# Performance work log

Hardware: AMD Instinct MI355X
Metric: run time of the kernel (lower is better)

Reference implementation:

```python
import jax, jax.numpy as jnp
import numpy as np

N_NODES = 100000
N_EDGES = 3200000
N_GRAPHS = 1024
HID = 64
NUM_CLASSES = 21


def setup_inputs() -> dict:
    key = jax.random.key(0)
    ks = jax.random.split(key, 12)
    x = jax.random.normal(ks[0], (N_NODES, 1), dtype=jnp.float32)
    edge_index = jax.random.randint(ks[1], (2, N_EDGES), 0, N_NODES, dtype=jnp.int64)
    batch = jnp.sort(jax.random.randint(ks[2], (N_NODES,), 0, N_GRAPHS, dtype=jnp.int64))
    def lin(k, fan_in, fan_out):
        bound = 1.0 / np.sqrt(fan_in)
        return jax.random.uniform(k, (fan_in, fan_out), jnp.float32, -bound, bound)
    return {
        "x": x,
        "edge_index": edge_index,
        "batch": batch,
        # SAGEConv1: lin_l (on aggregated neighbors, with bias), lin_r (root, no bias)
        "W1l": lin(ks[3], 1, HID), "b1": jnp.zeros((HID,), jnp.float32), "W1r": lin(ks[4], 1, HID),
        # SAGEConv2
        "W2l": lin(ks[5], HID, HID), "b2": jnp.zeros((HID,), jnp.float32), "W2r": lin(ks[6], HID, HID),
        # classifier
        "Wc": lin(ks[7], HID, NUM_CLASSES), "bc": jnp.zeros((NUM_CLASSES,), jnp.float32),
    }


def _sage_conv(x, src, dst, Wl, bl, Wr):
    # mean-aggregate neighbor features: gather from src, scatter-mean to dst
    msg = x[src]                                              # [E, F] gather
    agg = jax.ops.segment_sum(msg, dst, num_segments=N_NODES)  # [N, F]
    cnt = jax.ops.segment_sum(jnp.ones((src.shape[0],), x.dtype), dst, num_segments=N_NODES)
    agg = agg / jnp.maximum(cnt, 1.0)[:, None]
    # out = lin_l(aggr) + lin_r(x)
    return agg @ Wl + bl + x @ Wr


def reference(x, edge_index, batch, W1l, b1, W1r, W2l, b2, W2r, Wc, bc):
    src, dst = edge_index[0], edge_index[1]
    h = jax.nn.relu(_sage_conv(x, src, dst, W1l, b1, W1r))
    h = jax.nn.relu(_sage_conv(h, src, dst, W2l, b2, W2r))
    # global mean pool over graphs
    pooled = jax.ops.segment_sum(h, batch, num_segments=N_GRAPHS)
    gcnt = jax.ops.segment_sum(jnp.ones((h.shape[0],), h.dtype), batch, num_segments=N_GRAPHS)
    pooled = pooled / jnp.maximum(gcnt, 1.0)[:, None]
    return pooled @ Wc + bc
```

## Files before the change

kernel.cpp:

```cpp
#include <hip/hip_runtime.h>

#define N_NODES 100000
#define N_EDGES 3200000
#define N_GRAPHS 1024
#define NCLS 21
#define NBKT 782
#define CAP 4480
#define NB 512
#define CHUNK 6250
#define TROW 72

typedef short s8v __attribute__((ext_vector_type(8)));
typedef float f4v __attribute__((ext_vector_type(4)));

__device__ __forceinline__ float bf2f(unsigned short u) {
    return __uint_as_float(((unsigned)u) << 16);
}
__device__ __forceinline__ unsigned short f2bf(float f) {
    unsigned u = __float_as_uint(f);
    unsigned r = 0x7fffu + ((u >> 16) & 1u);
    return (unsigned short)((u + r) >> 16);
}
__device__ __forceinline__ float lo2f(unsigned w) { return __uint_as_float(w << 16); }
__device__ __forceinline__ float hi2f(unsigned w) { return __uint_as_float(w & 0xffff0000u); }

__global__ void k_prep(const float* __restrict__ W2l, const float* __restrict__ W2r,
                       unsigned short* __restrict__ wp,
                       const int* __restrict__ batch, int* __restrict__ gstart,
                       int* __restrict__ gcur) {
    if (blockIdx.x < 32) {
        int tid = blockIdx.x * 256 + threadIdx.x;
        int frag = tid >> 9;
        int r = tid & 511;
        int L = r >> 3, j = r & 7;
        int kstep = frag >> 2, nt = frag & 3;
        int k = kstep * 32 + (L >> 4) * 8 + j;
        int n = nt * 16 + (L & 15);
        float val = (k < 64) ? W2l[k * 64 + n] : W2r[(k - 64) * 64 + n];
        wp[tid] = f2bf(val);
    } else if (blockIdx.x < 37) {
        int g = (blockIdx.x - 32) * 256 + threadIdx.x;
        if (g > N_GRAPHS) return;
        if (g == N_GRAPHS) { gstart[N_GRAPHS] = N_NODES; return; }
        int lo = 0, hi = N_NODES;
        while (lo < hi) { int m = (lo + hi) >> 1; if (batch[m] < g) lo = m + 1; else hi = m; }
        gstart[g] = lo;
    } else {
        for (int i = threadIdx.x; i < NBKT; i += 256) gcur[i] = i * CAP;
    }
}

__global__ __launch_bounds__(256) void k_binone(const int* __restrict__ src,
                                                const int* __restrict__ dst,
                                                int* __restrict__ gcur,
                                                unsigned int* __restrict__ bins) {
    __shared__ unsigned int ebuf[CHUNK];
    __shared__ unsigned short bbuf[CHUNK];
    __shared__ int lh[NBKT];
    __shared__ int lbase[NBKT];
    int t = threadIdx.x;
    for (int i = t; i < NBKT; i += 256) lh[i] = 0;
    __syncthreads();
    const int2* s2 = (const int2*)(src + blockIdx.x * CHUNK);
    const int2* d2 = (const int2*)(dst + blockIdx.x * CHUNK);
    for (int i = t; i < CHUNK / 2; i += 256) {
        int2 s = s2[i];
        int2 d = d2[i];
        uint2 pp;
        pp.x = ((unsigned)s.x << 7) | (unsigned)(d.x & 127);
        pp.y = ((unsigned)s.y << 7) | (unsigned)(d.y & 127);
        *(uint2*)(&ebuf[2 * i]) = pp;
        bbuf[2 * i]     = (unsigned short)(d.x >> 7);
        bbuf[2 * i + 1] = (unsigned short)(d.y >> 7);
        atomicAdd(&lh[d.x >> 7], 1);
        atomicAdd(&lh[d.y >> 7], 1);
    }
    __syncthreads();
    for (int i = t; i < NBKT; i += 256)
        lbase[i] = atomicAdd(&gcur[i], lh[i]);
    __syncthreads();
    for (int i = t; i < NBKT; i += 256) lh[i] = lbase[i];
    __syncthreads();
    for (int i = t; i < CHUNK; i += 256) {
        int b = (int)bbuf[i];
        int pos = atomicAdd(&lh[b], 1);
        if (pos < (b + 1) * CAP) bins[pos] = ebuf[i];
    }
}

__global__ __launch_bounds__(256) void k_build(
    const int* __restrict__ gcur, unsigned int* __restrict__ bins,
    int* __restrict__ row, unsigned short* __restrict__ deg,
    const float* __restrict__ x,
    const float* __restrict__ W1l, const float* __restrict__ b1,
    const float* __restrict__ W1r, unsigned short* __restrict__ h1b) {
    __shared__ unsigned int ebuf[CAP];
    __shared__ int hist[128];
    __shared__ int curs[128];
    __shared__ int lds[128];
    __shared__ float t1[128];
    int k = blockIdx.x, t = threadIdx.x;
    int e0 = k * CAP;
    int cnt = min(gcur[k] - e0, CAP);
    if (t < 128) { hist[t] = 0; t1[t] = 0.0f; }
    __syncthreads();
    for (int i = t; i < cnt; i += 256) {
        unsigned p = bins[e0 + i];
        ebuf[i] = p;
        atomicAdd(&hist[p & 127u], 1);
    }
    __syncthreads();
    if (t < 128) lds[t] = hist[t];
    __syncthreads();
    for (int off = 1; off < 128; off <<= 1) {
        int cur = (t < 128) ? lds[t] : 0;
        int add = (t < 128 && t >= off) ? lds[t - off] : 0;
        __syncthreads();
        if (t < 128) lds[t] = cur + add;
        __syncthreads();
    }
    if (t < 128) {
        int run = e0 + lds[t] - hist[t];
        curs[t] = run;
        int n = k * 128 + t;
        if (n < N_NODES) { row[n] = run; deg[n] = (unsigned short)hist[t]; }
    }
    __syncthreads();
    for (int i = t; i < cnt; i += 256) {
        unsigned p = ebuf[i];
        int slot = (int)(p & 127u);
        int pos = atomicAdd(&curs[slot], 1);
        bins[pos] = p >> 7;
        atomicAdd(&t1[slot], x[p >> 7]);
    }
    __syncthreads();
    for (int i = t; i < 128 * 64; i += 256) {
        int slot = i >> 6, f = i & 63;
        int n = k * 128 + slot;
        if (n >= N_NODES) break;
        float a = t1[slot] / fmaxf((float)hist[slot], 1.0f);
        float v = a * W1l[f] + b1[f] + x[n] * W1r[f];
        h1b[(size_t)n * 64 + f] = f2bf(fmaxf(v, 0.0f));
    }
}

__global__ __launch_bounds__(256) void k_l2f(
    const int* __restrict__ row, const unsigned short* __restrict__ deg,
    const unsigned int* __restrict__ csr,
    const unsigned short* __restrict__ h1b,
    const unsigned short* __restrict__ wp, const float* __restrict__ b2,
    unsigned short* __restrict__ h2b) {
    __shared__ unsigned short tile[4][16 * TROW];
    int wid = threadIdx.x >> 6;
    int w = blockIdx.x * 4 + wid;
    if (w >= N_NODES / 16) return;
    int L = threadIdx.x & 63;
    int fo = L & 7;
    int es = L >> 3;
    int fown = fo * 8 + es;
    unsigned short* tw = tile[wid];

    for (int t = 0; t < 16; t++) {
        int n = w * 16 + t;
        int r0 = row[n];
        int dn = (int)deg[n];
        int r1 = r0 + dn;
        float a0 = 0.f, a1 = 0.f, a2 = 0.f, a3 = 0.f,
              a4 = 0.f, a5 = 0.f, a6 = 0.f, a7 = 0.f;
        int base = r0;
        for (; base + 32 <= r1; base += 32) {
            int sA = (int)csr[base + es];
            int sB = (int)csr[base + 8 + es];
            int sC = (int)csr[base + 16 + es];
            int sD = (int)csr[base + 24 + es];
            uint4 dA = *(const uint4*)(h1b + (size_t)sA * 64 + fo * 8);
            uint4 dB = *(const uint4*)(h1b + (size_t)sB * 64 + fo * 8);
            uint4 dC = *(const uint4*)(h1b + (size_t)sC * 64 + fo * 8);
            uint4 dD = *(const uint4*)(h1b + (size_t)sD * 64 + fo * 8);
            a0 += lo2f(dA.x); a1 += hi2f(dA.x); a2 += lo2f(dA.y); a3 += hi2f(dA.y);
            a4 += lo2f(dA.z); a5 += hi2f(dA.z); a6 += lo2f(dA.w); a7 += hi2f(dA.w);
            a0 += lo2f(dB.x); a1 += hi2f(dB.x); a2 += lo2f(dB.y); a3 += hi2f(dB.y);
            a4 += lo2f(dB.z); a5 += hi2f(dB.z); a6 += lo2f(dB.w); a7 += hi2f(dB.w);
            a0 += lo2f(dC.x); a1 += hi2f(dC.x); a2 += lo2f(dC.y); a3 += hi2f(dC.y);
            a4 += lo2f(dC.z); a5 += hi2f(dC.z); a6 += lo2f(dC.w); a7 += hi2f(dC.w);
            a0 += lo2f(dD.x); a1 += hi2f(dD.x); a2 += lo2f(dD.y); a3 += hi2f(dD.y);
            a4 += lo2f(dD.z); a5 += hi2f(dD.z); a6 += lo2f(dD.w); a7 += hi2f(dD.w);
        }
        for (; base + 16 <= r1; base += 16) {
            int sA = (int)csr[base + es];
            int sB = (int)csr[base + 8 + es];
            uint4 dA = *(const uint4*)(h1b + (size_t)sA * 64 + fo * 8);
            uint4 dB = *(const uint4*)(h1b + (size_t)sB * 64 + fo * 8);
            a0 += lo2f(dA.x); a1 += hi2f(dA.x); a2 += lo2f(dA.y); a3 += hi2f(dA.y);
            a4 += lo2f(dA.z); a5 += hi2f(dA.z); a6 += lo2f(dA.w); a7 += hi2f(dA.w);
            a0 += lo2f(dB.x); a1 += hi2f(dB.x); a2 += lo2f(dB.y); a3 += hi2f(dB.y);
            a4 += lo2f(dB.z); a5 += hi2f(dB.z); a6 += lo2f(dB.w); a7 += hi2f(dB.w);
        }
        for (; base < r1; base += 8) {
            int e = base + es;
            bool act = e < r1;
            int sA = (int)csr[act ? e : r1 - 1];
            uint4 d = *(const uint4*)(h1b + (size_t)sA * 64 + fo * 8);
            unsigned m = act ? 0xffffffffu : 0u;
            d.x &= m; d.y &= m; d.z &= m; d.w &= m;
            a0 += lo2f(d.x); a1 += hi2f(d.x); a2 += lo2f(d.y); a3 += hi2f(d.y);
            a4 += lo2f(d.z); a5 += hi2f(d.z); a6 += lo2f(d.w); a7 += hi2f(d.w);
        }
        {
            bool hi = (es & 4) != 0;
            float s0 = hi ? a0 : a4, s1 = hi ? a1 : a5, s2 = hi ? a2 : a6, s3 = hi ? a3 : a7;
            float r0v = __shfl_xor(s0, 32, 64);
            float r1v = __shfl_xor(s1, 32, 64);
            float r2v = __shfl_xor(s2, 32, 64);
            float r3v = __shfl_xor(s3, 32, 64);
            a0 = (hi ? a4 : a0) + r0v;
            a1 = (hi ? a5 : a1) + r1v;
            a2 = (hi ? a6 : a2) + r2v;
            a3 = (hi ? a7 : a3) + r3v;
        }
        {
            bool hi = (es & 2) != 0;
            float s0 = hi ? a0 : a2, s1 = hi ? a1 : a3;
            float r0v = __shfl_xor(s0, 16, 64);
            float r1v = __shfl_xor(s1, 16, 64);
            a0 = (hi ? a2 : a0) + r0v;
            a1 = (hi ? a3 : a1) + r1v;
        }
        {
            bool hi = (es & 1) != 0;
            float s0 = hi ? a0 : a1;
            float r0v = __shfl_xor(s0, 8, 64);
            a0 = (hi ? a1 : a0) + r0v;
        }
        float inv = 1.0f / fmaxf((float)dn, 1.0f);
        tw[t * TROW + fown] = f2bf(a0 * inv);
    }

    int m = L & 15, q = L >> 4;
    int nrow = w * 16 + m;

    const s8v a0 = *(const s8v*)(tw + m * TROW + q * 8);
    const s8v a1 = *(const s8v*)(tw + m * TROW + 32 + q * 8);
    const s8v a2 = *(const s8v*)(h1b + (size_t)nrow * 64 + q * 8);
    const s8v a3 = *(const s8v*)(h1b + (size_t)nrow * 64 + 32 + q * 8);

#define LOADB(i) s8v B##i = *(const s8v*)(wp + (i) * 512 + L * 8)
    LOADB(0); LOADB(1); LOADB(2); LOADB(3);
    LOADB(4); LOADB(5); LOADB(6); LOADB(7);
    LOADB(8); LOADB(9); LOADB(10); LOADB(11);
    LOADB(12); LOADB(13); LOADB(14); LOADB(15);
#undef LOADB

    f4v acc0 = {0.f, 0.f, 0.f, 0.f}, acc1 = acc0, acc2 = acc0, acc3 = acc0;
    acc0 = __builtin_amdgcn_mfma_f32_16x16x32_bf16(a0, B0,  acc0, 0, 0, 0);
    acc0 = __builtin_amdgcn_mfma_f32_16x16x32_bf16(a1, B4,  acc0, 0, 0, 0);
    acc0 = __builtin_amdgcn_mfma_f32_16x16x32_bf16(a2, B8,  acc0, 0, 0, 0);
    acc0 = __builtin_amdgcn_mfma_f32_16x16x32_bf16(a3, B12, acc0, 0, 0, 0);
    acc1 = __builtin_amdgcn_mfma_f32_16x16x32_bf16(a0, B1,  acc1, 0, 0, 0);
    acc1 = __builtin_amdgcn_mfma_f32_16x16x32_bf16(a1, B5,  acc1, 0, 0, 0);
    acc1 = __builtin_amdgcn_mfma_f32_16x16x32_bf16(a2, B9,  acc1, 0, 0, 0);
    acc1 = __builtin_amdgcn_mfma_f32_16x16x32_bf16(a3, B13, acc1, 0, 0, 0);
    acc2 = __builtin_amdgcn_mfma_f32_16x16x32_bf16(a0, B2,  acc2, 0, 0, 0);
    acc2 = __builtin_amdgcn_mfma_f32_16x16x32_bf16(a1, B6,  acc2, 0, 0, 0);
    acc2 = __builtin_amdgcn_mfma_f32_16x16x32_bf16(a2, B10, acc2, 0, 0, 0);
    acc2 = __builtin_amdgcn_mfma_f32_16x16x32_bf16(a3, B14, acc2, 0, 0, 0);
    acc3 = __builtin_amdgcn_mfma_f32_16x16x32_bf16(a0, B3,  acc3, 0, 0, 0);
    acc3 = __builtin_amdgcn_mfma_f32_16x16x32_bf16(a1, B7,  acc3, 0, 0, 0);
    acc3 = __builtin_amdgcn_mfma_f32_16x16x32_bf16(a2, B11, acc3, 0, 0, 0);
    acc3 = __builtin_amdgcn_mfma_f32_16x16x32_bf16(a3, B15, acc3, 0, 0, 0);

    int fcol = L & 15;
    float bia0 = b2[fcol], bia1 = b2[16 + fcol], bia2 = b2[32 + fcol], bia3 = b2[48 + fcol];
    int rbase = w * 16 + q * 4;
#pragma unroll
    for (int r = 0; r < 4; r++) {
        size_t o = (size_t)(rbase + r) * 64 + fcol;
        h2b[o]      = f2bf(fmaxf(acc0[r] + bia0, 0.0f));
        h2b[o + 16] = f2bf(fmaxf(acc1[r] + bia1, 0.0f));
        h2b[o + 32] = f2bf(fmaxf(acc2[r] + bia2, 0.0f));
        h2b[o + 48] = f2bf(fmaxf(acc3[r] + bia3, 0.0f));
    }
}

__global__ __launch_bounds__(256) void k_head(
    const unsigned short* __restrict__ h2b, const int* __restrict__ gstart,
    const float* __restrict__ Wc, const float* __restrict__ bc,
    float* __restrict__ out) {
    __shared__ float part[4][64];
    __shared__ float rowv[64];
    int g = blockIdx.x;
    int wid = threadIdx.x >> 6;
    int f = threadIdx.x & 63;
    int ns = gstart[g], ne = gstart[g + 1];
    float s = 0.0f;
    int n = ns + wid;
    for (; n + 12 < ne; n += 16) {
        float v0 = bf2f(h2b[(size_t)(n)      * 64 + f]);
        float v1 = bf2f(h2b[(size_t)(n + 4)  * 64 + f]);
        float v2 = bf2f(h2b[(size_t)(n + 8)  * 64 + f]);
        float v3 = bf2f(h2b[(size_t)(n + 12) * 64 + f]);
        s += (v0 + v1) + (v2 + v3);
    }
    for (; n < ne; n += 4) s += bf2f(h2b[(size_t)n * 64 + f]);
    part[wid][f] = s;
    __syncthreads();
    if (threadIdx.x < 64) {
        float tot = part[0][f] + part[1][f] + part[2][f] + part[3][f];
        rowv[f] = tot / fmaxf((float)(ne - ns), 1.0f);
    }
    __syncthreads();
    if (threadIdx.x < NCLS) {
        float acc = bc[threadIdx.x];
#pragma unroll
        for (int kk = 0; kk < 64; kk++) acc += rowv[kk] * Wc[kk * NCLS + threadIdx.x];
        out[g * NCLS + threadIdx.x] = acc;
    }
}

extern "C" void kernel_launch(void* const* d_in, const int* in_sizes, int n_in,
                              void* d_out, int out_size, void* d_ws, size_t ws_size,
                              hipStream_t stream) {
    const float* x     = (const float*)d_in[0];
    const int*   eidx  = (const int*)d_in[1];
    const int*   batch = (const int*)d_in[2];
    const float* W1l   = (const float*)d_in[3];
    const float* b1    = (const float*)d_in[4];
    const float* W1r   = (const float*)d_in[5];
    const float* W2l   = (const float*)d_in[6];
    const float* b2    = (const float*)d_in[7];
    const float* W2r   = (const float*)d_in[8];
    const float* Wc    = (const float*)d_in[9];
    const float* bc    = (const float*)d_in[10];
    float* out = (float*)d_out;

    const int* src = eidx;
    const int* dst = eidx + N_EDGES;

    char* p = (char*)d_ws;
    unsigned int* bins  = (unsigned int*)p;     p += (size_t)NBKT * CAP * 4;
    unsigned short* h1b = (unsigned short*)p;   p += (size_t)N_NODES * 64 * 2;
    unsigned short* h2b = (unsigned short*)p;   p += (size_t)N_NODES * 64 * 2;
    int* row   = (int*)p;                       p += (size_t)(N_NODES + 1) * 4;
    unsigned short* deg = (unsigned short*)p;   p += (size_t)N_NODES * 2;
    int* gcur  = (int*)p;                       p += NBKT * 4;
    int* gstart= (int*)p;                       p += (N_GRAPHS + 1) * 4;
    unsigned short* wp = (unsigned short*)p;    p += 8192 * 2;

    k_prep  <<<38, 256, 0, stream>>>(W2l, W2r, wp, batch, gstart, gcur);
    k_binone<<<NB, 256, 0, stream>>>(src, dst, gcur, bins);
    k_build <<<NBKT, 256, 0, stream>>>(gcur, bins, row, deg, x, W1l, b1, W1r, h1b);
    k_l2f   <<<(N_NODES / 16 + 3) / 4, 256, 0, stream>>>(row, deg, bins, h1b, wp, b2, h2b);
    k_head  <<<N_GRAPHS, 256, 0, stream>>>(h2b, gstart, Wc, bc, out);
}
```

Before: 229.4 us.

## Split each 16-node tile across two waves in layer-2 aggregation and MFMA

The layer-2 kernel now has two waves share each 16-node tile. Each wave aggregates 8 nodes and then computes half of the 64 output columns with MFMA after a block barrier, so the grid doubles and per-wave serial gather latency halves. Row offsets and degrees for the 8 nodes are prefetched up front, and the bf16 unpack and accumulate now uses float2 vectors, which may allow packed adds. The cost is a __syncthreads in every block and duplicated A-operand loads across the two waves.

```diff
diff --git a/kernel.cpp b/kernel.cpp
--- a/kernel.cpp
+++ b/kernel.cpp
@@ -12,6 +12,7 @@
 
 typedef short s8v __attribute__((ext_vector_type(8)));
 typedef float f4v __attribute__((ext_vector_type(4)));
+typedef float f2v __attribute__((ext_vector_type(2)));
 
 __device__ __forceinline__ float bf2f(unsigned short u) {
     return __uint_as_float(((unsigned)u) << 16);
@@ -23,6 +24,12 @@
 }
 __device__ __forceinline__ float lo2f(unsigned w) { return __uint_as_float(w << 16); }
 __device__ __forceinline__ float hi2f(unsigned w) { return __uint_as_float(w & 0xffff0000u); }
+__device__ __forceinline__ f2v up2(unsigned w) {
+    f2v r;
+    r.x = __uint_as_float(w << 16);
+    r.y = __uint_as_float(w & 0xffff0000u);
+    return r;
+}
 
 __global__ void k_prep(const float* __restrict__ W2l, const float* __restrict__ W2r,
                        unsigned short* __restrict__ wp,
@@ -150,23 +157,30 @@
     const unsigned short* __restrict__ h1b,
     const unsigned short* __restrict__ wp, const float* __restrict__ b2,
     unsigned short* __restrict__ h2b) {
-    __shared__ unsigned short tile[4][16 * TROW];
+    __shared__ unsigned short tile[2][16 * TROW];
     int wid = threadIdx.x >> 6;
-    int w = blockIdx.x * 4 + wid;
-    if (w >= N_NODES / 16) return;
+    int pair = wid >> 1, half = wid & 1;
+    int tb = (blockIdx.x * 2 + pair) * 16;
+    if (tb >= N_NODES) return;
     int L = threadIdx.x & 63;
     int fo = L & 7;
     int es = L >> 3;
     int fown = fo * 8 + es;
-    unsigned short* tw = tile[wid];
-
-    for (int t = 0; t < 16; t++) {
-        int n = w * 16 + t;
-        int r0 = row[n];
-        int dn = (int)deg[n];
+    unsigned short* tw = tile[pair];
+
+    int r0a[8]; int dna[8];
+#pragma unroll
+    for (int t = 0; t < 8; t++) {
+        int n = tb + half * 8 + t;
+        r0a[t] = row[n];
+        dna[t] = (int)deg[n];
+    }
+
+    for (int t = 0; t < 8; t++) {
+        int r0 = r0a[t];
+        int dn = dna[t];
         int r1 = r0 + dn;
-        float a0 = 0.f, a1 = 0.f, a2 = 0.f, a3 = 0.f,
-              a4 = 0.f, a5 = 0.f, a6 = 0.f, a7 = 0.f;
+        f2v p0 = {0.f, 0.f}, p1 = p0, p2 = p0, p3 = p0;
         int base = r0;
         for (; base + 32 <= r1; base += 32) {
             int sA = (int)csr[base + es];
@@ -177,24 +191,18 @@
             uint4 dB = *(const uint4*)(h1b + (size_t)sB * 64 + fo * 8);
             uint4 dC = *(const uint4*)(h1b + (size_t)sC * 64 + fo * 8);
             uint4 dD = *(const uint4*)(h1b + (size_t)sD * 64 + fo * 8);
-            a0 += lo2f(dA.x); a1 += hi2f(dA.x); a2 += lo2f(dA.y); a3 += hi2f(dA.y);
-            a4 += lo2f(dA.z); a5 += hi2f(dA.z); a6 += lo2f(dA.w); a7 += hi2f(dA.w);
-            a0 += lo2f(dB.x); a1 += hi2f(dB.x); a2 += lo2f(dB.y); a3 += hi2f(dB.y);
-            a4 += lo2f(dB.z); a5 += hi2f(dB.z); a6 += lo2f(dB.w); a7 += hi2f(dB.w);
-            a0 += lo2f(dC.x); a1 += hi2f(dC.x); a2 += lo2f(dC.y); a3 += hi2f(dC.y);
-            a4 += lo2f(dC.z); a5 += hi2f(dC.z); a6 += lo2f(dC.w); a7 += hi2f(dC.w);
-            a0 += lo2f(dD.x); a1 += hi2f(dD.x); a2 += lo2f(dD.y); a3 += hi2f(dD.y);
-            a4 += lo2f(dD.z); a5 += hi2f(dD.z); a6 += lo2f(dD.w); a7 += hi2f(dD.w);
+            p0 += up2(dA.x); p1 += up2(dA.y); p2 += up2(dA.z); p3 += up2(dA.w);
+            p0 += up2(dB.x); p1 += up2(dB.y); p2 += up2(dB.z); p3 += up2(dB.w);
+            p0 += up2(dC.x); p1 += up2(dC.y); p2 += up2(dC.z); p3 += up2(dC.w);
+            p0 += up2(dD.x); p1 += up2(dD.y); p2 += up2(dD.z); p3 += up2(dD.w);
         }
         for (; base + 16 <= r1; base += 16) {
             int sA = (int)csr[base + es];
             int sB = (int)csr[base + 8 + es];
             uint4 dA = *(const uint4*)(h1b + (size_t)sA * 64 + fo * 8);
             uint4 dB = *(const uint4*)(h1b + (size_t)sB * 64 + fo * 8);
-            a0 += lo2f(dA.x); a1 += hi2f(dA.x); a2 += lo2f(dA.y); a3 += hi2f(dA.y);
-            a4 += lo2f(dA.z); a5 += hi2f(dA.z); a6 += lo2f(dA.w); a7 += hi2f(dA.w);
-            a0 += lo2f(dB.x); a1 += hi2f(dB.x); a2 += lo2f(dB.y); a3 += hi2f(dB.y);
-            a4 += lo2f(dB.z); a5 += hi2f(dB.z); a6 += lo2f(dB.w); a7 += hi2f(dB.w);
+            p0 += up2(dA.x); p1 += up2(dA.y); p2 += up2(dA.z); p3 += up2(dA.w);
+            p0 += up2(dB.x); p1 += up2(dB.y); p2 += up2(dB.z); p3 += up2(dB.w);
         }
         for (; base < r1; base += 8) {
             int e = base + es;
@@ -203,82 +211,73 @@
             uint4 d = *(const uint4*)(h1b + (size_t)sA * 64 + fo * 8);
             unsigned m = act ? 0xffffffffu : 0u;
             d.x &= m; d.y &= m; d.z &= m; d.w &= m;
-            a0 += lo2f(d.x); a1 += hi2f(d.x); a2 += lo2f(d.y); a3 += hi2f(d.y);
-            a4 += lo2f(d.z); a5 += hi2f(d.z); a6 += lo2f(d.w); a7 += hi2f(d.w);
+            p0 += up2(d.x); p1 += up2(d.y); p2 += up2(d.z); p3 += up2(d.w);
         }
         {
             bool hi = (es & 4) != 0;
-            float s0 = hi ? a0 : a4, s1 = hi ? a1 : a5, s2 = hi ? a2 : a6, s3 = hi ? a3 : a7;
-            float r0v = __shfl_xor(s0, 32, 64);
-            float r1v = __shfl_xor(s1, 32, 64);
-            float r2v = __shfl_xor(s2, 32, 64);
-            float r3v = __shfl_xor(s3, 32, 64);
-            a0 = (hi ? a4 : a0) + r0v;
-            a1 = (hi ? a5 : a1) + r1v;
-            a2 = (hi ? a6 : a2) + r2v;
-            a3 = (hi ? a7 : a3) + r3v;
+            f2v s0 = hi ? p0 : p2, s1 = hi ? p1 : p3;
+            f2v r0v, r1v;
+            r0v.x = __shfl_xor(s0.x, 32, 64); r0v.y = __shfl_xor(s0.y, 32, 64);
+            r1v.x = __shfl_xor(s1.x, 32, 64); r1v.y = __shfl_xor(s1.y, 32, 64);
+            p0 = (hi ? p2 : p0) + r0v;
+            p1 = (hi ? p3 : p1) + r1v;
         }
         {
             bool hi = (es & 2) != 0;
-            float s0 = hi ? a0 : a2, s1 = hi ? a1 : a3;
-            float r0v = __shfl_xor(s0, 16, 64);
-            float r1v = __shfl_xor(s1, 16, 64);
-            a0 = (hi ? a2 : a0) + r0v;
-            a1 = (hi ? a3 : a1) + r1v;
-        }
+            f2v s0 = hi ? p0 : p1;
+            f2v rv;
+            rv.x = __shfl_xor(s0.x, 16, 64); rv.y = __shfl_xor(s0.y, 16, 64);
+            p0 = (hi ? p1 : p0) + rv;
+        }
+        float a0;
         {
             bool hi = (es & 1) != 0;
-            float s0 = hi ? a0 : a1;
-            float r0v = __shfl_xor(s0, 8, 64);
-            a0 = (hi ? a1 : a0) + r0v;
+            float s = hi ? p0.x : p0.y;
+            float rv = __shfl_xor(s, 8, 64);
+            a0 = (hi ? p0.y : p0.x) + rv;
         }
         float inv = 1.0f / fmaxf((float)dn, 1.0f);
-        tw[t * TROW + fown] = f2bf(a0 * inv);
-    }
+        tw[(half * 8 + t) * TROW + fown] = f2bf(a0 * inv);
+    }
+    __syncthreads();
 
     int m = L & 15, q = L >> 4;
-    int nrow = w * 16 + m;
+    int nrow = tb + m;
 
     const s8v a0 = *(const s8v*)(tw + m * TROW + q * 8);
     const s8v a1 = *(const s8v*)(tw + m * TROW + 32 + q * 8);
     const s8v a2 = *(const s8v*)(h1b + (size_t)nrow * 64 + q * 8);
     const s8v a3 = *(const s8v*)(h1b + (size_t)nrow * 64 + 32 + q * 8);
 
-#define LOADB(i) s8v B##i = *(const s8v*)(wp + (i) * 512 + L * 8)
-    LOADB(0); LOADB(1); LOADB(2); LOADB(3);
-    LOADB(4); LOADB(5); LOADB(6); LOADB(7);
-    LOADB(8); LOADB(9); LOADB(10); LOADB(11);
-    LOADB(12); LOADB(13); LOADB(14); LOADB(15);
-#undef LOADB
-
-    f4v acc0 = {0.f, 0.f, 0.f, 0.f}, acc1 = acc0, acc2 = acc0, acc3 = acc0;
-    acc0 = __builtin_amdgcn_mfma_f32_16x16x32_bf16(a0, B0,  acc0, 0, 0, 0);
-    acc0 = __builtin_amdgcn_mfma_f32_16x16x32_bf16(a1, B4,  acc0, 0, 0, 0);
-    acc0 = __builtin_amdgcn_mfma_f32_16x16x32_bf16(a2, B8,  acc0, 0, 0, 0);
-    acc0 = __builtin_amdgcn_mfma_f32_16x16x32_bf16(a3, B12, acc0, 0, 0, 0);
-    acc1 = __builtin_amdgcn_mfma_f32_16x16x32_bf16(a0, B1,  acc1, 0, 0, 0);
-    acc1 = __builtin_amdgcn_mfma_f32_16x16x32_bf16(a1, B5,  acc1, 0, 0, 0);
-    acc1 = __builtin_amdgcn_mfma_f32_16x16x32_bf16(a2, B9,  acc1, 0, 0, 0);
+    int nt0 = half * 2, nt1 = nt0 + 1;
+    const unsigned short* wpb = wp + (size_t)L * 8;
+    s8v B00 = *(const s8v*)(wpb + (size_t)(nt0)      * 512);
+    s8v B01 = *(const s8v*)(wpb + (size_t)(nt0 + 4)  * 512);
+    s8v B02 = *(const s8v*)(wpb + (size_t)(nt0 + 8)  * 512);
+    s8v B03 = *(const s8v*)(wpb + (size_t)(nt0 + 12) * 512);
+    s8v B10 = *(const s8v*)(wpb + (size_t)(nt1)      * 512);
+    s8v B11 = *(const s8v*)(wpb + (size_t)(nt1 + 4)  * 512);
+    s8v B12 = *(const s8v*)(wpb + (size_t)(nt1 + 8)  * 512);
+    s8v B13 = *(const s8v*)(wpb + (size_t)(nt1 + 12) * 512);
+
+    f4v acc0 = {0.f, 0.f, 0.f, 0.f}, acc1 = acc0;
+    acc0 = __builtin_amdgcn_mfma_f32_16x16x32_bf16(a0, B00, acc0, 0, 0, 0);
+    acc0 = __builtin_amdgcn_mfma_f32_16x16x32_bf16(a1, B01, acc0, 0, 0, 0);
+    acc0 = __builtin_amdgcn_mfma_f32_16x16x32_bf16(a2, B02, acc0, 0, 0, 0);
+    acc0 = __builtin_amdgcn_mfma_f32_16x16x32_bf16(a3, B03, acc0, 0, 0, 0);
+    acc1 = __builtin_amdgcn_mfma_f32_16x16x32_bf16(a0, B10, acc1, 0, 0, 0);
+    acc1 = __builtin_amdgcn_mfma_f32_16x16x32_bf16(a1, B11, acc1, 0, 0, 0);
+    acc1 = __builtin_amdgcn_mfma_f32_16x16x32_bf16(a2, B12, acc1, 0, 0, 0);
     acc1 = __builtin_amdgcn_mfma_f32_16x16x32_bf16(a3, B13, acc1, 0, 0, 0);
-    acc2 = __builtin_amdgcn_mfma_f32_16x16x32_bf16(a0, B2,  acc2, 0, 0, 0);
-    acc2 = __builtin_amdgcn_mfma_f32_16x16x32_bf16(a1, B6,  acc2, 0, 0, 0);
-    acc2 = __builtin_amdgcn_mfma_f32_16x16x32_bf16(a2, B10, acc2, 0, 0, 0);
-    acc2 = __builtin_amdgcn_mfma_f32_16x16x32_bf16(a3, B14, acc2, 0, 0, 0);
-    acc3 = __builtin_amdgcn_mfma_f32_16x16x32_bf16(a0, B3,  acc3, 0, 0, 0);
-    acc3 = __builtin_amdgcn_mfma_f32_16x16x32_bf16(a1, B7,  acc3, 0, 0, 0);
-    acc3 = __builtin_amdgcn_mfma_f32_16x16x32_bf16(a2, B11, acc3, 0, 0, 0);
-    acc3 = __builtin_amdgcn_mfma_f32_16x16x32_bf16(a3, B15, acc3, 0, 0, 0);
 
     int fcol = L & 15;
-    float bia0 = b2[fcol], bia1 = b2[16 + fcol], bia2 = b2[32 + fcol], bia3 = b2[48 + fcol];
-    int rbase = w * 16 + q * 4;
+    float bia0 = b2[nt0 * 16 + fcol], bia1 = b2[nt1 * 16 + fcol];
+    int rbase = tb + q * 4;
 #pragma unroll
     for (int r = 0; r < 4; r++) {
         size_t o = (size_t)(rbase + r) * 64 + fcol;
-        h2b[o]      = f2bf(fmaxf(acc0[r] + bia0, 0.0f));
-        h2b[o + 16] = f2bf(fmaxf(acc1[r] + bia1, 0.0f));
-        h2b[o + 32] = f2bf(fmaxf(acc2[r] + bia2, 0.0f));
-        h2b[o + 48] = f2bf(fmaxf(acc3[r] + bia3, 0.0f));
+        h2b[o + nt0 * 16] = f2bf(fmaxf(acc0[r] + bia0, 0.0f));
+        h2b[o + nt1 * 16] = f2bf(fmaxf(acc1[r] + bia1, 0.0f));
     }
 }
 
@@ -349,6 +348,6 @@
     k_prep  <<<38, 256, 0, stream>>>(W2l, W2r, wp, batch, gstart, gcur);
     k_binone<<<NB, 256, 0, stream>>>(src, dst, gcur, bins);
     k_build <<<NBKT, 256, 0, stream>>>(gcur, bins, row, deg, x, W1l, b1, W1r, h1b);
-    k_l2f   <<<(N_NODES / 16 + 3) / 4, 256, 0, stream>>>(row, deg, bins, h1b, wp, b2, h2b);
+    k_l2f   <<<(N_NODES / 32), 256, 0, stream>>>(row, deg, bins, h1b, wp, b2, h2b);
     k_head  <<<N_GRAPHS, 256, 0, stream>>>(h2b, gstart, Wc, bc, out);
 }
```

Result: no change. 231.7 us (+1.0%).

## Process eight nodes per wave concurrently in layer-2 aggregation with swizzled indices

Applied to the files above, without the earlier changes.

The layer-2 neighbor gather now assigns each group of 8 lanes its own node, processing 8 nodes in parallel over two passes instead of one node at a time across the whole wave. Edge indices are loaded once per 8-lane group and broadcast with ds_swizzle, and the next batch of indices is prefetched. Packed float2 accumulation is used. This removes the cross-lane shuffle reduction and the per-node serialization but introduces divergence when degrees differ between the 8 nodes sharing a wave.

```diff
diff --git a/kernel.cpp b/kernel.cpp
--- a/kernel.cpp
+++ b/kernel.cpp
@@ -12,6 +12,7 @@
 
 typedef short s8v __attribute__((ext_vector_type(8)));
 typedef float f4v __attribute__((ext_vector_type(4)));
+typedef float f2v __attribute__((ext_vector_type(2)));
 
 __device__ __forceinline__ float bf2f(unsigned short u) {
     return __uint_as_float(((unsigned)u) << 16);
@@ -21,8 +22,12 @@
     unsigned r = 0x7fffu + ((u >> 16) & 1u);
     return (unsigned short)((u + r) >> 16);
 }
-__device__ __forceinline__ float lo2f(unsigned w) { return __uint_as_float(w << 16); }
-__device__ __forceinline__ float hi2f(unsigned w) { return __uint_as_float(w & 0xffff0000u); }
+__device__ __forceinline__ f2v up2(unsigned w) {
+    f2v r;
+    r.x = __uint_as_float(w << 16);
+    r.y = __uint_as_float(w & 0xffff0000u);
+    return r;
+}
 
 __global__ void k_prep(const float* __restrict__ W2l, const float* __restrict__ W2r,
                        unsigned short* __restrict__ wp,
@@ -156,85 +161,60 @@
     if (w >= N_NODES / 16) return;
     int L = threadIdx.x & 63;
     int fo = L & 7;
-    int es = L >> 3;
-    int fown = fo * 8 + es;
+    int g  = L >> 3;
     unsigned short* tw = tile[wid];
 
-    for (int t = 0; t < 16; t++) {
-        int n = w * 16 + t;
-        int r0 = row[n];
-        int dn = (int)deg[n];
+    int nA = w * 16 + g;
+    int nB = nA + 8;
+    int r0A = row[nA]; int dnA = (int)deg[nA];
+    int r0B = row[nB]; int dnB = (int)deg[nB];
+
+#define SWZ(v, j) __builtin_amdgcn_ds_swizzle((v), (((j) << 5) | 0x18))
+#define GA(j, dj) { int sj = SWZ(idx, j); \
+                    dj = *(const uint4*)(h1b + (size_t)(unsigned)sj * 64 + fo * 8); }
+#define AC(dj) { p0 += up2(dj.x); p1 += up2(dj.y); p2 += up2(dj.z); p3 += up2(dj.w); }
+#define REM(j) if ((j) < rem) { int sj = SWZ(idx, j); \
+                    uint4 d = *(const uint4*)(h1b + (size_t)(unsigned)sj * 64 + fo * 8); \
+                    AC(d) }
+
+#pragma unroll
+    for (int pass = 0; pass < 2; pass++) {
+        int r0 = pass ? r0B : r0A;
+        int dn = pass ? dnB : dnA;
+        int trow = g + 8 * pass;
         int r1 = r0 + dn;
-        float a0 = 0.f, a1 = 0.f, a2 = 0.f, a3 = 0.f,
-              a4 = 0.f, a5 = 0.f, a6 = 0.f, a7 = 0.f;
+        f2v p0 = {0.f, 0.f}, p1 = p0, p2 = p0, p3 = p0;
         int base = r0;
-        for (; base + 32 <= r1; base += 32) {
-            int sA = (int)csr[base + es];
-            int sB = (int)csr[base + 8 + es];
-            int sC = (int)csr[base + 16 + es];
-            int sD = (int)csr[base + 24 + es];
-            uint4 dA = *(const uint4*)(h1b + (size_t)sA * 64 + fo * 8);
-            uint4 dB = *(const uint4*)(h1b + (size_t)sB * 64 + fo * 8);
-            uint4 dC = *(const uint4*)(h1b + (size_t)sC * 64 + fo * 8);
-            uint4 dD = *(const uint4*)(h1b + (size_t)sD * 64 + fo * 8);
-            a0 += lo2f(dA.x); a1 += hi2f(dA.x); a2 += lo2f(dA.y); a3 += hi2f(dA.y);
-            a4 += lo2f(dA.z); a5 += hi2f(dA.z); a6 += lo2f(dA.w); a7 += hi2f(dA.w);
-            a0 += lo2f(dB.x); a1 += hi2f(dB.x); a2 += lo2f(dB.y); a3 += hi2f(dB.y);
-            a4 += lo2f(dB.z); a5 += hi2f(dB.z); a6 += lo2f(dB.w); a7 += hi2f(dB.w);
-            a0 += lo2f(dC.x); a1 += hi2f(dC.x); a2 += lo2f(dC.y); a3 += hi2f(dC.y);
-            a4 += lo2f(dC.z); a5 += hi2f(dC.z); a6 += lo2f(dC.w); a7 += hi2f(dC.w);
-            a0 += lo2f(dD.x); a1 += hi2f(dD.x); a2 += lo2f(dD.y); a3 += hi2f(dD.y);
-            a4 += lo2f(dD.z); a5 += hi2f(dD.z); a6 += lo2f(dD.w); a7 += hi2f(dD.w);
+        int idx = (int)csr[min(base + fo, r1 - 1)];
+        while (base + 8 <= r1) {
+            int nb = base + 8;
+            int idxn = (int)csr[min(nb + fo, r1 - 1)];
+            uint4 d0, d1, d2, d3, d4, d5, d6, d7;
+            GA(0, d0) GA(1, d1) GA(2, d2) GA(3, d3)
+            GA(4, d4) GA(5, d5) GA(6, d6) GA(7, d7)
+            idx = idxn;
+            AC(d0) AC(d1) AC(d2) AC(d3)
+            AC(d4) AC(d5) AC(d6) AC(d7)
+            base = nb;
         }
-        for (; base + 16 <= r1; base += 16) {
-            int sA = (int)csr[base + es];
-            int sB = (int)csr[base + 8 + es];
-            uint4 dA = *(const uint4*)(h1b + (size_t)sA * 64 + fo * 8);
-            uint4 dB = *(const uint4*)(h1b + (size_t)sB * 64 + fo * 8);
-            a0 += lo2f(dA.x); a1 += hi2f(dA.x); a2 += lo2f(dA.y); a3 += hi2f(dA.y);
-            a4 += lo2f(dA.z); a5 += hi2f(dA.z); a6 += lo2f(dA.w); a7 += hi2f(dA.w);
-            a0 += lo2f(dB.x); a1 += hi2f(dB.x); a2 += lo2f(dB.y); a3 += hi2f(dB.y);
-            a4 += lo2f(dB.z); a5 += hi2f(dB.z); a6 += lo2f(dB.w); a7 += hi2f(dB.w);
-        }
-        for (; base < r1; base += 8) {
-            int e = base + es;
-            bool act = e < r1;
-            int sA = (int)csr[act ? e : r1 - 1];
-            uint4 d = *(const uint4*)(h1b + (size_t)sA * 64 + fo * 8);
-            unsigned m = act ? 0xffffffffu : 0u;
-            d.x &= m; d.y &= m; d.z &= m; d.w &= m;
-            a0 += lo2f(d.x); a1 += hi2f(d.x); a2 += lo2f(d.y); a3 += hi2f(d.y);
-            a4 += lo2f(d.z); a5 += hi2f(d.z); a6 += lo2f(d.w); a7 += hi2f(d.w);
-        }
-        {
-            bool hi = (es & 4) != 0;
-            float s0 = hi ? a0 : a4, s1 = hi ? a1 : a5, s2 = hi ? a2 : a6, s3 = hi ? a3 : a7;
-            float r0v = __shfl_xor(s0, 32, 64);
-            float r1v = __shfl_xor(s1, 32, 64);
-            float r2v = __shfl_xor(s2, 32, 64);
-            float r3v = __shfl_xor(s3, 32, 64);
-            a0 = (hi ? a4 : a0) + r0v;
-            a1 = (hi ? a5 : a1) + r1v;
-            a2 = (hi ? a6 : a2) + r2v;
-            a3 = (hi ? a7 : a3) + r3v;
-        }
-        {
-            bool hi = (es & 2) != 0;
-            float s0 = hi ? a0 : a2, s1 = hi ? a1 : a3;
-            float r0v = __shfl_xor(s0, 16, 64);
-            float r1v = __shfl_xor(s1, 16, 64);
-            a0 = (hi ? a2 : a0) + r0v;
-            a1 = (hi ? a3 : a1) + r1v;
-        }
-        {
-            bool hi = (es & 1) != 0;
-            float s0 = hi ? a0 : a1;
-            float r0v = __shfl_xor(s0, 8, 64);
-            a0 = (hi ? a1 : a0) + r0v;
+        int rem = r1 - base;
+        if (rem > 0) {
+            REM(0) REM(1) REM(2) REM(3)
+            REM(4) REM(5) REM(6) REM(7)
         }
         float inv = 1.0f / fmaxf((float)dn, 1.0f);
-        tw[t * TROW + fown] = f2bf(a0 * inv);
-    }
+        p0 *= inv; p1 *= inv; p2 *= inv; p3 *= inv;
+        unsigned w0 = (unsigned)f2bf(p0.x) | ((unsigned)f2bf(p0.y) << 16);
+        unsigned w1 = (unsigned)f2bf(p1.x) | ((unsigned)f2bf(p1.y) << 16);
+        unsigned w2 = (unsigned)f2bf(p2.x) | ((unsigned)f2bf(p2.y) << 16);
+        unsigned w3 = (unsigned)f2bf(p3.x) | ((unsigned)f2bf(p3.y) << 16);
+        uint4 pk; pk.x = w0; pk.y = w1; pk.z = w2; pk.w = w3;
+        *(uint4*)(tw + trow * TROW + fo * 8) = pk;
+    }
+#undef SWZ
+#undef GA
+#undef AC
+#undef REM
 
     int m = L & 15, q = L >> 4;
     int nrow = w * 16 + m;
```

New measurement: 234.1 us. +2.0%, slower.
